# Optimization experiments

Hardware: AMD Instinct MI355X
Metric: run time of the kernel (lower is better)

## Reference

```python
import jax, jax.numpy as jnp
import numpy as np

N = 100000
E = 1600000
IN_DIM = 128
HID_DIM = 128
NUM_CLASSES = 40


def setup_inputs() -> dict:
    key = jax.random.key(0)
    k1, k2, k3, k4, k5, k6 = jax.random.split(key, 6)
    x = jax.random.normal(k1, (N, IN_DIM), dtype=jnp.float32)
    e = jax.random.randint(k2, (2, E), 0, N, dtype=jnp.int64)
    s1 = 1.0 / np.sqrt(IN_DIM)
    s2 = 1.0 / np.sqrt(HID_DIM)
    W1 = jax.random.uniform(k3, (IN_DIM, HID_DIM), jnp.float32, -s1, s1)
    b1 = jax.random.uniform(k4, (HID_DIM,), jnp.float32, -s1, s1)
    W2 = jax.random.uniform(k5, (HID_DIM, NUM_CLASSES), jnp.float32, -s2, s2)
    b2 = jax.random.uniform(k6, (NUM_CLASSES,), jnp.float32, -s2, s2)
    return {"x": x, "e": e, "W1": W1, "b1": b1, "W2": W2, "b2": b2}


def _gcn_conv(x, src, dst, norm, W, b, n):
    # linear transform first (PyG GCNConv), then normalized aggregation
    h = x @ W                                    # [N, d_out]
    out = jax.ops.segment_sum(h[src] * norm[:, None], dst, num_segments=n)
    return out + b


def reference(x, e, W1, b1, W2, b2):
    n = x.shape[0]
    loop = jnp.arange(n, dtype=e.dtype)
    src = jnp.concatenate([e[0], loop])          # add self-loops
    dst = jnp.concatenate([e[1], loop])
    deg = jax.ops.segment_sum(jnp.ones_like(dst, dtype=x.dtype), dst, num_segments=n)
    d_inv_sqrt = deg ** -0.5                     # deg >= 1 due to self-loops
    norm = d_inv_sqrt[src] * d_inv_sqrt[dst]     # symmetric normalization
    h = jax.nn.relu(_gcn_conv(x, src, dst, norm, W1, b1, n))
    return _gcn_conv(h, src, dst, norm, W2, b2, n)
```

## Files before the change

kernel.cpp:

```cpp
#include <hip/hip_runtime.h>


typedef unsigned int u32;
typedef unsigned short u16;
typedef __attribute__((ext_vector_type(8))) short short8;
typedef __attribute__((ext_vector_type(4))) float floatx4;

#define CHUNK 4096

static __device__ inline u16 f2bf(float f) {
    u32 u = __float_as_uint(f);
    return (u16)((u + 0x7FFFu + ((u >> 16) & 1u)) >> 16);
}
static __device__ inline u32 pack2(float a, float b) {
    return (u32)f2bf(a) | ((u32)f2bf(b) << 16);
}
static __device__ inline float bflo(u32 u) { return __uint_as_float(u << 16); }
static __device__ inline float bfhi(u32 u) { return __uint_as_float(u & 0xffff0000u); }

static __device__ inline bool detect_is64(const int* e32, int lane) {
    bool nz = e32[2 * lane + 1] != 0;
    return __ballot(nz) == 0ull;
}

__global__ void k_prepW(const float* __restrict__ W1, const float* __restrict__ W2,
                        u16* __restrict__ WTb, u16* __restrict__ W2Tb) {
    int id = blockIdx.x * 256 + threadIdx.x;
    if (id < 16384) {
        int k = id >> 7, c = id & 127;
        WTb[c * 128 + k] = f2bf(W1[id]);
    } else {
        int id2 = id - 16384;
        if (id2 < 6144) {
            int c = id2 >> 7, k = id2 & 127;
            W2Tb[id2] = f2bf(c < 40 ? W2[k * 40 + c] : 0.f);
        }
    }
}

__global__ __launch_bounds__(256) void k_front(const void* __restrict__ e_raw,
                                               int E, int NC, int NB,
                                               int* __restrict__ histG,
                                               const float* __restrict__ X,
                                               const u16* __restrict__ WTb,
                                               u16* __restrict__ H1s, int n) {
    __shared__ u32 smem[64 * 68 + 128 * 68];
    const int tid = threadIdx.x;
    if ((int)blockIdx.x < NC) {
        int* h = (int*)smem;
        h[tid] = 0; h[tid + 256] = 0;
        __syncthreads();
        const int* e32 = (const int*)e_raw;
        bool is64 = detect_is64(e32, tid & 63);
        int c = blockIdx.x;
        int j0 = c * CHUNK, j1 = min(E, j0 + CHUNK);
        for (int j = j0 + tid; j < j1; j += 256) {
            int d = is64 ? (int)((const long long*)e_raw)[E + j] : e32[E + j];
            atomicAdd(&h[d >> 8], 1);
        }
        __syncthreads();
        for (int b = tid; b < NB; b += 256) histG[(size_t)b * NC + c] = h[b];
        return;
    }
    u32* As = smem;
    u32* Bs = smem + 64 * 68;
    const int row0 = ((int)blockIdx.x - NC) * 64;
#pragma unroll
    for (int it = 0; it < 8; it++) {
        int i = tid + it * 256;
        int r = i >> 5;
        int c4 = (i & 31) << 2;
        int gr = row0 + r;
        float4 v = make_float4(0.f, 0.f, 0.f, 0.f);
        if (gr < n) v = *(const float4*)(X + (size_t)gr * 128 + c4);
        uint2 p;
        p.x = pack2(v.x, v.y);
        p.y = pack2(v.z, v.w);
        *(uint2*)&As[r * 68 + (c4 >> 1)] = p;
    }
#pragma unroll
    for (int it = 0; it < 8; it++) {
        int i = tid + it * 256;
        int r = i >> 4;
        int c4 = (i & 15) << 2;
        *(uint4*)&Bs[r * 68 + c4] =
            *(const uint4*)((const u32*)WTb + (size_t)r * 64 + c4);
    }
    __syncthreads();

    const int lane = tid & 63;
    const int wave = tid >> 6;
    const int wr = wave >> 1;
    const int wc = wave & 1;
    const int mrow = lane & 15;
    const int quad = lane >> 4;

    floatx4 acc[2][4] = {};
    for (int k0 = 0; k0 < 128; k0 += 32) {
        int koff = (k0 >> 1) + quad * 4;
        short8 a[2], b[4];
#pragma unroll
        for (int i = 0; i < 2; i++)
            a[i] = *(const short8*)&As[((wr * 2 + i) * 16 + mrow) * 68 + koff];
#pragma unroll
        for (int j = 0; j < 4; j++)
            b[j] = *(const short8*)&Bs[((wc * 4 + j) * 16 + mrow) * 68 + koff];
#pragma unroll
        for (int i = 0; i < 2; i++)
#pragma unroll
            for (int j = 0; j < 4; j++)
                acc[i][j] = __builtin_amdgcn_mfma_f32_16x16x32_bf16(
                    a[i], b[j], acc[i][j], 0, 0, 0);
    }
#pragma unroll
    for (int i = 0; i < 2; i++) {
        int gr0 = row0 + (wr * 2 + i) * 16 + quad * 4;
#pragma unroll
        for (int j = 0; j < 4; j++) {
            int gcol = (wc * 4 + j) * 16 + mrow;
#pragma unroll
            for (int rg = 0; rg < 4; rg++) {
                int grow = gr0 + rg;
                if (grow < n)
                    H1s[(size_t)grow * 128 + gcol] = f2bf(acc[i][j][rg]);
            }
        }
    }
}

__global__ void k_scan1(const int* __restrict__ in, int* __restrict__ out,
                        int* __restrict__ bsum, int n) {
    __shared__ int sh[256];
    int i = blockIdx.x * 256 + threadIdx.x;
    int v = (i < n) ? in[i] : 0;
    sh[threadIdx.x] = v;
    __syncthreads();
    for (int off = 1; off < 256; off <<= 1) {
        int t = (threadIdx.x >= off) ? sh[threadIdx.x - off] : 0;
        __syncthreads();
        sh[threadIdx.x] += t;
        __syncthreads();
    }
    if (i < n) out[i] = sh[threadIdx.x] - v;
    if (threadIdx.x == 255) bsum[blockIdx.x] = sh[255];
}

__global__ void k_scan2(int* __restrict__ bsum, int nb) {
    __shared__ int sh[1024];
    int t = threadIdx.x;
    int v = (t < nb) ? bsum[t] : 0;
    sh[t] = v;
    __syncthreads();
    for (int off = 1; off < 1024; off <<= 1) {
        int u = (t >= off) ? sh[t - off] : 0;
        __syncthreads();
        sh[t] += u;
        __syncthreads();
    }
    if (t < nb) bsum[t] = sh[t] - v;
}

__global__ __launch_bounds__(256) void k_place(const void* __restrict__ e_raw,
                                               const int* __restrict__ histOff,
                                               const int* __restrict__ bsumH,
                                               u32* __restrict__ tmp,
                                               int E, int NB, int NC) {
    __shared__ int cur[512];
    int c = blockIdx.x;
    int t = threadIdx.x;
    for (int b = t; b < NB; b += 256) {
        int idx = b * NC + c;
        cur[b] = histOff[idx] + bsumH[idx >> 8];
    }
    __syncthreads();
    const int* e32 = (const int*)e_raw;
    bool is64 = detect_is64(e32, t & 63);
    int j0 = c * CHUNK, j1 = min(E, j0 + CHUNK);
    for (int j = j0 + t; j < j1; j += 256) {
        int s, d;
        if (is64) {
            s = (int)((const long long*)e_raw)[j];
            d = (int)((const long long*)e_raw)[E + j];
        } else {
            s = e32[j];
            d = e32[E + j];
        }
        int pos = atomicAdd(&cur[d >> 8], 1);
        tmp[pos] = (u32)s | ((u32)(d & 255) << 24);
    }
}

__global__ __launch_bounds__(256) void k_degsort(const u32* __restrict__ tmp,
                                                 const int* __restrict__ histOff,
                                                 const int* __restrict__ bsumH,
                                                 int* __restrict__ degI,
                                                 float* __restrict__ dinv,
                                                 int* __restrict__ rs,
                                                 int* __restrict__ eSrc,
                                                 int n, int NB, int NC, int E) {
    __shared__ int cnt[256];
    __shared__ int sh[256];
    __shared__ int cur[256];
    int b = blockIdx.x;
    int t = threadIdx.x;
    cnt[t] = 0;
    __syncthreads();
    int i0 = b * NC;
    int seg0 = histOff[i0] + bsumH[i0 >> 8];
    int seg1 = E;
    if (b + 1 < NB) {
        int i1 = (b + 1) * NC;
        seg1 = histOff[i1] + bsumH[i1 >> 8];
    }
    for (int j = seg0 + t; j < seg1; j += 256) atomicAdd(&cnt[tmp[j] >> 24], 1);
    __syncthreads();
    int v = cnt[t];
    sh[t] = v;
    __syncthreads();
    for (int off = 1; off < 256; off <<= 1) {
        int u = (t >= off) ? sh[t - off] : 0;
        __syncthreads();
        sh[t] += u;
        __syncthreads();
    }
    int myStart = seg0 + sh[t] - v;
    cur[t] = myStart;
    int node = b * 256 + t;
    if (node < n) {
        degI[node] = v;
        dinv[node] = rsqrtf((float)v + 1.0f);
        rs[node] = myStart;
    }
    __syncthreads();
    for (int j = seg0 + t; j < seg1; j += 256) {
        u32 rec = tmp[j];
        int dl = rec >> 24;
        int s = (int)(rec & 0x00FFFFFFu);
        int pos = atomicAdd(&cur[dl], 1);
        eSrc[pos] = s;
    }
}

__global__ __launch_bounds__(256) void k_gather128(
    const u32* __restrict__ Hb, const int* __restrict__ rs,
    const int* __restrict__ degI, const int* __restrict__ eSrc,
    const float* __restrict__ dinv, const float* __restrict__ b1,
    u32* __restrict__ outb, int n) {
    int wave = threadIdx.x >> 6;
    int lane = threadIdx.x & 63;
    int node = blockIdx.x * 4 + wave;
    if (node >= n) return;
    int start = rs[node];
    int deg = degI[node];
    float ax = 0.f, ay = 0.f;
    for (int base = 0; base < deg; base += 64) {
        int mS = 0;
        float mW = 0.f;
        if (base + lane < deg) { mS = eSrc[start + base + lane]; mW = dinv[mS]; }
        int cnt = min(64, deg - base);
        int t = 0;
        for (; t + 16 <= cnt; t += 16) {
            int ss[16];
            float ww[16];
            u32 uu[16];
#pragma unroll
            for (int q = 0; q < 16; q++) {
                ss[q] = __shfl(mS, t + q);
                ww[q] = __shfl(mW, t + q);
            }
#pragma unroll
            for (int q = 0; q < 16; q++) uu[q] = Hb[(size_t)ss[q] * 64 + lane];
#pragma unroll
            for (int q = 0; q < 16; q++) {
                ax = fmaf(ww[q], bflo(uu[q]), ax);
                ay = fmaf(ww[q], bfhi(uu[q]), ay);
            }
        }
        for (; t + 4 <= cnt; t += 4) {
            int s0 = __shfl(mS, t + 0), s1 = __shfl(mS, t + 1);
            int s2 = __shfl(mS, t + 2), s3 = __shfl(mS, t + 3);
            float w0 = __shfl(mW, t + 0), w1 = __shfl(mW, t + 1);
            float w2 = __shfl(mW, t + 2), w3 = __shfl(mW, t + 3);
            u32 u0 = Hb[(size_t)s0 * 64 + lane];
            u32 u1 = Hb[(size_t)s1 * 64 + lane];
            u32 u2 = Hb[(size_t)s2 * 64 + lane];
            u32 u3 = Hb[(size_t)s3 * 64 + lane];
            ax = fmaf(w0, bflo(u0), ax); ay = fmaf(w0, bfhi(u0), ay);
            ax = fmaf(w1, bflo(u1), ax); ay = fmaf(w1, bfhi(u1), ay);
            ax = fmaf(w2, bflo(u2), ax); ay = fmaf(w2, bfhi(u2), ay);
            ax = fmaf(w3, bflo(u3), ax); ay = fmaf(w3, bfhi(u3), ay);
        }
        for (; t < cnt; t++) {
            int s = __shfl(mS, t);
            float w = __shfl(mW, t);
            u32 u = Hb[(size_t)s * 64 + lane];
            ax = fmaf(w, bflo(u), ax); ay = fmaf(w, bfhi(u), ay);
        }
    }
    float di = dinv[node];
    u32 us = Hb[(size_t)node * 64 + lane];
    float inx = fmaf(di, bflo(us), ax);
    float iny = fmaf(di, bfhi(us), ay);
    float2 bv = *(const float2*)(b1 + lane * 2);
    float rx = fmaxf(fmaf(di, inx, bv.x), 0.f);
    float ry = fmaxf(fmaf(di, iny, bv.y), 0.f);
    outb[(size_t)node * 64 + lane] = pack2(rx, ry);
}

__global__ __launch_bounds__(256) void k_gemm2(const u32* __restrict__ A1b,
                                               const u16* __restrict__ W2Tb,
                                               const float* __restrict__ dinv,
                                               u16* __restrict__ H2s, int n) {
    __shared__ u32 As[64 * 68];
    __shared__ u32 Bs[48 * 68];
    const int tid = threadIdx.x;
    const int row0 = blockIdx.x * 64;
#pragma unroll
    for (int it = 0; it < 4; it++) {
        int i = tid + it * 256;
        int r = i >> 4;
        int c4 = (i & 15) << 2;
        int gr = row0 + r;
        uint4 v = make_uint4(0u, 0u, 0u, 0u);
        if (gr < n) v = *(const uint4*)(A1b + (size_t)gr * 64 + c4);
        *(uint4*)&As[r * 68 + c4] = v;
    }
#pragma unroll
    for (int it = 0; it < 3; it++) {
        int i = tid + it * 256;
        int r = i >> 4;
        int c4 = (i & 15) << 2;
        *(uint4*)&Bs[r * 68 + c4] =
            *(const uint4*)((const u32*)W2Tb + (size_t)r * 64 + c4);
    }
    __syncthreads();

    const int lane = tid & 63;
    const int wave = tid >> 6;
    const int mrow = lane & 15;
    const int quad = lane >> 4;

    floatx4 acc[3] = {};
    for (int k0 = 0; k0 < 128; k0 += 32) {
        int koff = (k0 >> 1) + quad * 4;
        short8 a = *(const short8*)&As[(wave * 16 + mrow) * 68 + koff];
#pragma unroll
        for (int j = 0; j < 3; j++) {
            short8 b = *(const short8*)&Bs[(j * 16 + mrow) * 68 + koff];
            acc[j] = __builtin_amdgcn_mfma_f32_16x16x32_bf16(a, b, acc[j], 0, 0, 0);
        }
    }
    int gr0 = row0 + wave * 16 + quad * 4;
    float dv[4];
#pragma unroll
    for (int rg = 0; rg < 4; rg++)
        dv[rg] = (gr0 + rg < n) ? dinv[gr0 + rg] : 0.f;
#pragma unroll
    for (int j = 0; j < 3; j++) {
        int gcol = j * 16 + mrow;
        if (gcol < 40) {
#pragma unroll
            for (int rg = 0; rg < 4; rg++) {
                int grow = gr0 + rg;
                if (grow < n)
                    H2s[(size_t)grow * 40 + gcol] = f2bf(dv[rg] * acc[j][rg]);
            }
        }
    }
}

__global__ __launch_bounds__(256) void k_gather40(
    const u32* __restrict__ H2b, const int* __restrict__ rs,
    const int* __restrict__ degI, const int* __restrict__ eSrc,
    const float* __restrict__ dinv, const float* __restrict__ b2,
    float* __restrict__ out, int n) {
    int wave = threadIdx.x >> 6;
    int lane = threadIdx.x & 63;
    int node = blockIdx.x * 4 + wave;
    if (node >= n) return;
    int start = rs[node];
    int deg = degI[node];
    int g = lane / 20;
    int l = lane - g * 20;
    float ax = 0.f, ay = 0.f;
    for (int base = 0; base < deg; base += 64) {
        int mS = 0;
        if (base + lane < deg) mS = eSrc[start + base + lane];
        int cnt = min(64, deg - base);
        for (int t = 0; t < cnt; t += 12) {
            int i0 = t + g, i1 = t + 3 + g, i2 = t + 6 + g, i3 = t + 9 + g;
            int s0 = __shfl(mS, i0 & 63), s1 = __shfl(mS, i1 & 63);
            int s2 = __shfl(mS, i2 & 63), s3 = __shfl(mS, i3 & 63);
            bool v0 = (g < 3) && (i0 < cnt), v1 = (g < 3) && (i1 < cnt);
            bool v2 = (g < 3) && (i2 < cnt), v3 = (g < 3) && (i3 < cnt);
            u32 u0 = H2b[(size_t)s0 * 20 + l];
            u32 u1 = H2b[(size_t)s1 * 20 + l];
            u32 u2 = H2b[(size_t)s2 * 20 + l];
            u32 u3 = H2b[(size_t)s3 * 20 + l];
            if (v0) { ax += bflo(u0); ay += bfhi(u0); }
            if (v1) { ax += bflo(u1); ay += bfhi(u1); }
            if (v2) { ax += bflo(u2); ay += bfhi(u2); }
            if (v3) { ax += bflo(u3); ay += bfhi(u3); }
        }
    }
    float x1 = __shfl(ax, (lane + 20) & 63), y1 = __shfl(ay, (lane + 20) & 63);
    float x2 = __shfl(ax, (lane + 40) & 63), y2 = __shfl(ay, (lane + 40) & 63);
    if (lane < 20) {
        float di = dinv[node];
        u32 u = H2b[(size_t)node * 20 + l];
        float2 bv = *(const float2*)(b2 + l * 2);
        float ox = fmaf(di, ax + x1 + x2 + bflo(u), bv.x);
        float oy = fmaf(di, ay + y1 + y2 + bfhi(u), bv.y);
        *(float2*)(out + (size_t)node * 40 + l * 2) = make_float2(ox, oy);
    }
}

extern "C" void kernel_launch(void* const* d_in, const int* in_sizes, int n_in,
                              void* d_out, int out_size, void* d_ws, size_t ws_size,
                              hipStream_t stream) {
    const float* x  = (const float*)d_in[0];
    const void*  e  = d_in[1];
    const float* W1 = (const float*)d_in[2];
    const float* b1 = (const float*)d_in[3];
    const float* W2 = (const float*)d_in[4];
    const float* b2 = (const float*)d_in[5];
    float* out = (float*)d_out;

    const int n = in_sizes[0] / 128;
    const int E = in_sizes[1] / 2;
    const int NB = (n + 255) / 256;
    const int NC = (E + CHUNK - 1) / CHUNK;
    const int NH = NB * NC;
    const int nbH = (NH + 255) / 256;
    const int G1 = (n + 63) / 64;

    int*   degI    = (int*)d_ws;
    int*   rs      = degI + n;
    int*   bsumH   = rs + n;
    float* dinv    = (float*)(bsumH + 1024);
    int*   histG   = (int*)(dinv + n);
    int*   histOff = histG + NH;
    size_t off = (size_t)((char*)(histOff + NH) - (char*)d_ws);
    off = (off + 15) & ~(size_t)15;
    u16*   WTb    = (u16*)((char*)d_ws + off);
    u16*   W2Tb   = WTb + 16384;
    off = (size_t)((char*)(W2Tb + 6144) - (char*)d_ws);
    off = (off + 15) & ~(size_t)15;
    u32*   tmp    = (u32*)((char*)d_ws + off);
    int*   eSrc   = (int*)(tmp + (size_t)E);
    u16*   H1s    = (u16*)(eSrc + (size_t)E);
    u32*   H1b    = (u32*)H1s;
    u32*   A1b    = (u32*)(H1s + (size_t)n * 128);
    u16*   H2s    = (u16*)(A1b + (size_t)n * 64);
    u32*   H2b    = (u32*)H2s;

    k_prepW<<<88, 256, 0, stream>>>(W1, W2, WTb, W2Tb);
    k_front<<<NC + G1, 256, 0, stream>>>(e, E, NC, NB, histG, x, WTb, H1s, n);

    k_scan1<<<nbH, 256, 0, stream>>>(histG, histOff, bsumH, NH);
    k_scan2<<<1, 1024, 0, stream>>>(bsumH, nbH);
    k_place<<<NC, 256, 0, stream>>>(e, histOff, bsumH, tmp, E, NB, NC);

    k_degsort<<<NB, 256, 0, stream>>>(tmp, histOff, bsumH, degI, dinv, rs,
                                      eSrc, n, NB, NC, E);

    k_gather128<<<(n + 3) / 4, 256, 0, stream>>>(H1b, rs, degI, eSrc, dinv,
                                                 b1, A1b, n);
    k_gemm2<<<(n + 63) / 64, 256, 0, stream>>>(A1b, W2Tb, dinv, H2s, n);
    k_gather40<<<(n + 3) / 4, 256, 0, stream>>>(H2b, rs, degI, eSrc, dinv,
                                                b2, out, n);
}
```

Measured before the change: 302.3 us.

## Store H1 in column-sliced layout and gather per feature slice

The first GEMM now writes H1 as 8 column slices of 16 bf16 features each, stored contiguously per slice. The layer-1 gather assigns each block one slice, so 8 lanes cover a 32-byte row segment and 8 neighbours are fetched in parallel per wave, with a shuffle reduction at the end. The aim is a much smaller per-slice working set that fits in cache better during random neighbour gathers, and more neighbours in flight per instruction. The cost is that the edge list and dinv are read 8 times, plus extra shuffle-reduction work and partial-width stores.

New measurement: 507.7 us. 1.68x slower.

```diff
diff --git a/kernel.cpp b/kernel.cpp
--- a/kernel.cpp
+++ b/kernel.cpp
@@ -117,12 +117,12 @@
         int gr0 = row0 + (wr * 2 + i) * 16 + quad * 4;
 #pragma unroll
         for (int j = 0; j < 4; j++) {
-            int gcol = (wc * 4 + j) * 16 + mrow;
+            u16* dst = H1s + (size_t)(wc * 4 + j) * ((size_t)n * 16);
 #pragma unroll
             for (int rg = 0; rg < 4; rg++) {
                 int grow = gr0 + rg;
                 if (grow < n)
-                    H1s[(size_t)grow * 128 + gcol] = f2bf(acc[i][j][rg]);
+                    dst[(size_t)grow * 16 + mrow] = f2bf(acc[i][j][rg]);
             }
         }
     }
@@ -246,65 +246,65 @@
     const int* __restrict__ degI, const int* __restrict__ eSrc,
     const float* __restrict__ dinv, const float* __restrict__ b1,
     u32* __restrict__ outb, int n) {
-    int wave = threadIdx.x >> 6;
-    int lane = threadIdx.x & 63;
-    int node = blockIdx.x * 4 + wave;
-    if (node >= n) return;
-    int start = rs[node];
-    int deg = degI[node];
-    float ax = 0.f, ay = 0.f;
-    for (int base = 0; base < deg; base += 64) {
-        int mS = 0;
-        float mW = 0.f;
-        if (base + lane < deg) { mS = eSrc[start + base + lane]; mW = dinv[mS]; }
-        int cnt = min(64, deg - base);
-        int t = 0;
-        for (; t + 16 <= cnt; t += 16) {
-            int ss[16];
-            float ww[16];
-            u32 uu[16];
-#pragma unroll
-            for (int q = 0; q < 16; q++) {
-                ss[q] = __shfl(mS, t + q);
-                ww[q] = __shfl(mW, t + q);
+    const int wave = threadIdx.x >> 6;
+    const int lane = threadIdx.x & 63;
+    const int slice = blockIdx.x & 7;
+    const int chunk = blockIdx.x >> 3;
+    const int g = lane >> 3;
+    const int l = lane & 7;
+    const u32* __restrict__ Hq = Hb + (size_t)slice * ((size_t)n * 8);
+    const float2 bv = *(const float2*)(b1 + (slice * 8 + l) * 2);
+
+    const int node0 = chunk * 16 + wave * 4;
+    for (int i = 0; i < 4; i++) {
+        int node = node0 + i;
+        if (node >= n) return;
+        int start = rs[node];
+        int deg = degI[node];
+        float ax = 0.f, ay = 0.f;
+        for (int base = 0; base < deg; base += 64) {
+            int mS = 0;
+            float mW = 0.f;
+            if (base + lane < deg) {
+                mS = __builtin_nontemporal_load(eSrc + start + base + lane);
+                mW = dinv[mS];
             }
-#pragma unroll
-            for (int q = 0; q < 16; q++) uu[q] = Hb[(size_t)ss[q] * 64 + lane];
-#pragma unroll
-            for (int q = 0; q < 16; q++) {
-                ax = fmaf(ww[q], bflo(uu[q]), ax);
-                ay = fmaf(ww[q], bfhi(uu[q]), ay);
+            int cnt = min(64, deg - base);
+            int t = 0;
+            for (; t + 16 <= cnt; t += 16) {
+                int s0 = __shfl(mS, t + g);
+                int s1 = __shfl(mS, t + 8 + g);
+                float w0 = __shfl(mW, t + g);
+                float w1 = __shfl(mW, t + 8 + g);
+                u32 u0 = Hq[(size_t)s0 * 8 + l];
+                u32 u1 = Hq[(size_t)s1 * 8 + l];
+                ax = fmaf(w0, bflo(u0), ax); ay = fmaf(w0, bfhi(u0), ay);
+                ax = fmaf(w1, bflo(u1), ax); ay = fmaf(w1, bfhi(u1), ay);
             }
-        }
-        for (; t + 4 <= cnt; t += 4) {
-            int s0 = __shfl(mS, t + 0), s1 = __shfl(mS, t + 1);
-            int s2 = __shfl(mS, t + 2), s3 = __shfl(mS, t + 3);
-            float w0 = __shfl(mW, t + 0), w1 = __shfl(mW, t + 1);
-            float w2 = __shfl(mW, t + 2), w3 = __shfl(mW, t + 3);
-            u32 u0 = Hb[(size_t)s0 * 64 + lane];
-            u32 u1 = Hb[(size_t)s1 * 64 + lane];
-            u32 u2 = Hb[(size_t)s2 * 64 + lane];
-            u32 u3 = Hb[(size_t)s3 * 64 + lane];
-            ax = fmaf(w0, bflo(u0), ax); ay = fmaf(w0, bfhi(u0), ay);
-            ax = fmaf(w1, bflo(u1), ax); ay = fmaf(w1, bfhi(u1), ay);
-            ax = fmaf(w2, bflo(u2), ax); ay = fmaf(w2, bfhi(u2), ay);
-            ax = fmaf(w3, bflo(u3), ax); ay = fmaf(w3, bfhi(u3), ay);
-        }
-        for (; t < cnt; t++) {
-            int s = __shfl(mS, t);
-            float w = __shfl(mW, t);
-            u32 u = Hb[(size_t)s * 64 + lane];
-            ax = fmaf(w, bflo(u), ax); ay = fmaf(w, bfhi(u), ay);
-        }
-    }
-    float di = dinv[node];
-    u32 us = Hb[(size_t)node * 64 + lane];
-    float inx = fmaf(di, bflo(us), ax);
-    float iny = fmaf(di, bfhi(us), ay);
-    float2 bv = *(const float2*)(b1 + lane * 2);
-    float rx = fmaxf(fmaf(di, inx, bv.x), 0.f);
-    float ry = fmaxf(fmaf(di, iny, bv.y), 0.f);
-    outb[(size_t)node * 64 + lane] = pack2(rx, ry);
+            for (; t < cnt; t += 8) {
+                int idx = t + g;
+                int s = __shfl(mS, idx & 63);
+                float w = __shfl(mW, idx & 63);
+                if (idx >= cnt) w = 0.f;
+                u32 u = Hq[(size_t)s * 8 + l];
+                ax = fmaf(w, bflo(u), ax);
+                ay = fmaf(w, bfhi(u), ay);
+            }
+        }
+        for (int off = 8; off < 64; off <<= 1) {
+            ax += __shfl_xor(ax, off);
+            ay += __shfl_xor(ay, off);
+        }
+        float di = dinv[node];
+        u32 us = Hq[(size_t)node * 8 + l];
+        float inx = fmaf(di, bflo(us), ax);
+        float iny = fmaf(di, bfhi(us), ay);
+        float rx = fmaxf(fmaf(di, inx, bv.x), 0.f);
+        float ry = fmaxf(fmaf(di, iny, bv.y), 0.f);
+        if (g == 0)
+            __builtin_nontemporal_store(
+                pack2(rx, ry), outb + (size_t)node * 64 + slice * 8 + l);
+    }
 }
 
 __global__ __launch_bounds__(256) void k_gemm2(const u32* __restrict__ A1b,
@@ -464,8 +464,8 @@
     k_degsort<<<NB, 256, 0, stream>>>(tmp, histOff, bsumH, degI, dinv, rs,
                                       eSrc, n, NB, NC, E);
 
-    k_gather128<<<(n + 3) / 4, 256, 0, stream>>>(H1b, rs, degI, eSrc, dinv,
-                                                 b1, A1b, n);
+    k_gather128<<<8 * ((n + 15) / 16), 256, 0, stream>>>(H1b, rs, degI, eSrc,
+                                                         dinv, b1, A1b, n);
     k_gemm2<<<(n + 63) / 64, 256, 0, stream>>>(A1b, W2Tb, dinv, H2s, n);
     k_gather40<<<(n + 3) / 4, 256, 0, stream>>>(H2b, rs, degI, eSrc, dinv,
                                                 b2, out, n);
```

## Split H2 into two 20-column slices and gather with per-node lane groups

Applied to the files above, without the earlier changes.

The layer-2 GEMM now writes H2 as two column slices of 20 bf16 (10 u32) each instead of one 40-wide row. The layer-2 gather launches two blocks per chunk, one per slice. Each wave handles 6 nodes with 10 lanes per node, and each node's lanes loop over edges with an 8-deep software-pipelined index prefetch and row loads. This replaces one wave per node with shuffle-based edge distribution, aiming to cut idle lanes and the cross-lane reduction, and to make each slice's working set more cache-friendly. In exchange, 4 of 64 lanes sit idle, and each node's source indices are read twice, once per slice.

After: 299.4 us. No clear change (-1.0%).

```diff
diff --git a/kernel.cpp b/kernel.cpp
--- a/kernel.cpp
+++ b/kernel.cpp
@@ -7,6 +7,9 @@
 typedef __attribute__((ext_vector_type(4))) float floatx4;
 
 #define CHUNK 4096
+
+#define REP7(M)  M(0) M(1) M(2) M(3) M(4) M(5) M(6)
+#define REP8(M)  M(0) M(1) M(2) M(3) M(4) M(5) M(6) M(7)
 
 static __device__ inline u16 f2bf(float f) {
     u32 u = __float_as_uint(f);
@@ -359,11 +362,14 @@
     for (int j = 0; j < 3; j++) {
         int gcol = j * 16 + mrow;
         if (gcol < 40) {
+            int sl = (gcol >= 20) ? 1 : 0;
+            int c = gcol - sl * 20;
+            u16* dstp = H2s + (size_t)sl * ((size_t)n * 20);
 #pragma unroll
             for (int rg = 0; rg < 4; rg++) {
                 int grow = gr0 + rg;
                 if (grow < n)
-                    H2s[(size_t)grow * 40 + gcol] = f2bf(dv[rg] * acc[j][rg]);
+                    dstp[(size_t)grow * 20 + c] = f2bf(dv[rg] * acc[j][rg]);
             }
         }
     }
@@ -374,45 +380,62 @@
     const int* __restrict__ degI, const int* __restrict__ eSrc,
     const float* __restrict__ dinv, const float* __restrict__ b2,
     float* __restrict__ out, int n) {
-    int wave = threadIdx.x >> 6;
-    int lane = threadIdx.x & 63;
-    int node = blockIdx.x * 4 + wave;
+    const int lane = threadIdx.x & 63;
+    const int wave = threadIdx.x >> 6;
+    const int g = lane / 10;
+    const int l = lane - g * 10;
+    const int slice = blockIdx.x & 1;
+    const int chunk = blockIdx.x >> 1;
+    if (g >= 6) return;
+    const u32* __restrict__ Hs = H2b + (size_t)slice * ((size_t)n * 10);
+
+    const int node = chunk * 24 + wave * 6 + g;
     if (node >= n) return;
-    int start = rs[node];
-    int deg = degI[node];
-    int g = lane / 20;
-    int l = lane - g * 20;
+    const int start = rs[node];
+    const int deg = degI[node];
     float ax = 0.f, ay = 0.f;
-    for (int base = 0; base < deg; base += 64) {
-        int mS = 0;
-        if (base + lane < deg) mS = eSrc[start + base + lane];
-        int cnt = min(64, deg - base);
-        for (int t = 0; t < cnt; t += 12) {
-            int i0 = t + g, i1 = t + 3 + g, i2 = t + 6 + g, i3 = t + 9 + g;
-            int s0 = __shfl(mS, i0 & 63), s1 = __shfl(mS, i1 & 63);
-            int s2 = __shfl(mS, i2 & 63), s3 = __shfl(mS, i3 & 63);
-            bool v0 = (g < 3) && (i0 < cnt), v1 = (g < 3) && (i1 < cnt);
-            bool v2 = (g < 3) && (i2 < cnt), v3 = (g < 3) && (i3 < cnt);
-            u32 u0 = H2b[(size_t)s0 * 20 + l];
-            u32 u1 = H2b[(size_t)s1 * 20 + l];
-            u32 u2 = H2b[(size_t)s2 * 20 + l];
-            u32 u3 = H2b[(size_t)s3 * 20 + l];
-            if (v0) { ax += bflo(u0); ay += bfhi(u0); }
-            if (v1) { ax += bflo(u1); ay += bfhi(u1); }
-            if (v2) { ax += bflo(u2); ay += bfhi(u2); }
-            if (v3) { ax += bflo(u3); ay += bfhi(u3); }
-        }
-    }
-    float x1 = __shfl(ax, (lane + 20) & 63), y1 = __shfl(ay, (lane + 20) & 63);
-    float x2 = __shfl(ax, (lane + 40) & 63), y2 = __shfl(ay, (lane + 40) & 63);
-    if (lane < 20) {
-        float di = dinv[node];
-        u32 u = H2b[(size_t)node * 20 + l];
-        float2 bv = *(const float2*)(b2 + l * 2);
-        float ox = fmaf(di, ax + x1 + x2 + bflo(u), bv.x);
-        float oy = fmaf(di, ay + y1 + y2 + bfhi(u), bv.y);
-        *(float2*)(out + (size_t)node * 40 + l * 2) = make_float2(ox, oy);
-    }
+    u32 r0, r1, r2, r3, r4, r5, r6, r7;
+    u32 u0, u1, u2, u3, u4, u5, u6, u7;
+    int t = 0;
+
+#define PH(K) u##K = Hs[(size_t)r##K * 10 + l];
+#define PF(K) r##K = (u32)eSrc[bq + K];
+#define PA(K) ax += bflo(u##K); ay += bfhi(u##K);
+
+    if (deg >= 8) {
+        int bq = start;
+        REP8(PF)
+        for (; t + 16 <= deg; t += 8) {
+            REP8(PH)
+            bq = start + t + 8;
+            REP8(PF)
+            REP8(PA)
+        }
+        REP8(PH)
+        REP8(PA)
+        t += 8;
+    }
+    if (t < deg) {
+        const int bq = start + t;
+        const int rm = deg - t - 1;
+#define PTF(K) r##K = (u32)eSrc[bq + min(K, rm)];
+#define PTA(K) if (K <= rm) { ax += bflo(u##K); ay += bfhi(u##K); }
+        REP7(PTF)
+        REP7(PH)
+        REP7(PTA)
+#undef PTF
+#undef PTA
+    }
+#undef PH
+#undef PF
+#undef PA
+    const float di = dinv[node];
+    const u32 us = Hs[(size_t)node * 10 + l];
+    const float2 bv = *(const float2*)(b2 + (slice * 10 + l) * 2);
+    float ox = fmaf(di, ax + bflo(us), bv.x);
+    float oy = fmaf(di, ay + bfhi(us), bv.y);
+    *(float2*)(out + (size_t)node * 40 + (slice * 10 + l) * 2) =
+        make_float2(ox, oy);
 }
 
 extern "C" void kernel_launch(void* const* d_in, const int* in_sizes, int n_in,
@@ -467,6 +490,6 @@
     k_gather128<<<(n + 3) / 4, 256, 0, stream>>>(H1b, rs, degI, eSrc, dinv,
                                                  b1, A1b, n);
     k_gemm2<<<(n + 63) / 64, 256, 0, stream>>>(A1b, W2Tb, dinv, H2s, n);
-    k_gather40<<<(n + 3) / 4, 256, 0, stream>>>(H2b, rs, degI, eSrc, dinv,
-                                                b2, out, n);
-}
+    k_gather40<<<2 * ((n + 23) / 24), 256, 0, stream>>>(H2b, rs, degI, eSrc,
+                                                        dinv, b2, out, n);
+}
```
